# Kernel tuning notes

Measured on AMD Instinct MI355X. Metric: run time of the kernel, lower is better.

## Reference

```python
import jax, jax.numpy as jnp
import numpy as np

D_MODEL = 256
N_HEADS = 8
N_LEVELS = 4
N_POINTS = 4
HEAD_DIM = D_MODEL // N_HEADS
SPATIAL = [(64, 64), (32, 32), (16, 16), (8, 8)]
LEN_IN = sum(h * w for h, w in SPATIAL)
BATCH = 4
LEN_Q = LEN_IN


def _offset_bias():
    # replicate the module's _reset_parameters grid init for sampling_offsets.bias
    th = np.arange(N_HEADS, dtype=np.float64) * (2.0 * np.pi / N_HEADS)
    g = np.stack([np.cos(th), np.sin(th)], -1)
    g = g / np.abs(g).max(-1, keepdims=True)
    g = np.tile(g[:, None, None, :], (1, N_LEVELS, N_POINTS, 1))
    g = g * (np.arange(N_POINTS) + 1)[None, None, :, None]
    return jnp.asarray(g.reshape(-1), jnp.float32)


def setup_inputs() -> dict:
    key = jax.random.key(0)
    ks = jax.random.split(key, 10)
    s = 1.0 / np.sqrt(D_MODEL)
    return {
        "query": jax.random.normal(ks[0], (BATCH, LEN_Q, D_MODEL), jnp.float32),
        "reference_points": jax.random.uniform(ks[1], (BATCH, LEN_Q, N_LEVELS, 2), jnp.float32),
        "input_flatten": jax.random.normal(ks[2], (BATCH, LEN_IN, D_MODEL), jnp.float32),
        "input_spatial_shapes": np.array(SPATIAL, dtype=np.int64),
        "input_level_start_index": np.cumsum([0] + [h * w for h, w in SPATIAL[:-1]]).astype(np.int64),
        "W_val": jax.random.normal(ks[3], (D_MODEL, D_MODEL), jnp.float32) * s,
        "b_val": jnp.zeros((D_MODEL,), jnp.float32),
        "W_off": jax.random.normal(ks[4], (D_MODEL, N_HEADS * N_LEVELS * N_POINTS * 2), jnp.float32) * 0.01,
        "b_off": _offset_bias(),
        "W_attn": jax.random.normal(ks[5], (D_MODEL, N_HEADS * N_LEVELS * N_POINTS), jnp.float32) * 0.01,
        "b_attn": jnp.zeros((N_HEADS * N_LEVELS * N_POINTS,), jnp.float32),
        "W_out": jax.random.normal(ks[6], (D_MODEL, D_MODEL), jnp.float32) * s,
        "b_out": jnp.zeros((D_MODEL,), jnp.float32),
    }


def bilinear_sample(v, grid):
    # v: [B, C, H, W]; grid: [B, Q, P, 2] normalized to [-1, 1] (x=W axis, y=H axis)
    # matches torch F.grid_sample(mode='bilinear', padding_mode='zeros', align_corners=False)
    B, C, H, W = v.shape
    x = (grid[..., 0] + 1.0) * (W * 0.5) - 0.5
    y = (grid[..., 1] + 1.0) * (H * 0.5) - 0.5
    x0 = jnp.floor(x)
    y0 = jnp.floor(y)
    wx = x - x0
    wy = y - y0
    v_flat = v.reshape(B, C, H * W)

    def corner(xi, yi, wgt):
        valid = (xi >= 0) & (xi <= W - 1) & (yi >= 0) & (yi <= H - 1)
        xc = jnp.clip(xi, 0, W - 1).astype(jnp.int32)
        yc = jnp.clip(yi, 0, H - 1).astype(jnp.int32)
        idx = (yc * W + xc).reshape(B, 1, -1)
        g = jnp.take_along_axis(v_flat, jnp.broadcast_to(idx, (B, C, idx.shape[-1])), axis=2)
        return g * (wgt * valid).reshape(B, 1, -1)

    out = (corner(x0, y0, (1 - wx) * (1 - wy))
           + corner(x0 + 1, y0, wx * (1 - wy))
           + corner(x0, y0 + 1, (1 - wx) * wy)
           + corner(x0 + 1, y0 + 1, wx * wy))
    return out.reshape(B, C, grid.shape[1], grid.shape[2])


def reference(query, reference_points, input_flatten, input_spatial_shapes,
              input_level_start_index, W_val, b_val, W_off, b_off,
              W_attn, b_attn, W_out, b_out):
    ss = np.asarray(input_spatial_shapes)  # static [L, 2] (H, W)
    Nb, Lq, _ = query.shape
    value = (input_flatten @ W_val + b_val).reshape(Nb, -1, N_HEADS, HEAD_DIM)
    off = (query @ W_off + b_off).reshape(Nb, Lq, N_HEADS, N_LEVELS, N_POINTS, 2)
    attn = (query @ W_attn + b_attn).reshape(Nb, Lq, N_HEADS, N_LEVELS * N_POINTS)
    attn = jax.nn.softmax(attn, -1).reshape(Nb, Lq, N_HEADS, N_LEVELS, N_POINTS)
    # offset normalizer: (W, H) per level
    normalizer = jnp.asarray(ss[:, ::-1].copy(), jnp.float32)
    loc = reference_points[:, :, None, :, None, :] + off / normalizer[None, None, None, :, None, :]
    grids = 2.0 * loc - 1.0  # [N, Lq, H, L, P, 2]
    splits = np.cumsum([int(h) * int(w) for h, w in ss])[:-1]
    value_list = jnp.split(value, splits, axis=1)
    out = jnp.zeros((Nb * N_HEADS, HEAD_DIM, Lq), query.dtype)
    for lid, (h, w) in enumerate(ss):
        h, w = int(h), int(w)
        v = value_list[lid].transpose(0, 2, 3, 1).reshape(Nb * N_HEADS, HEAD_DIM, h, w)
        g = grids[:, :, :, lid].transpose(0, 2, 1, 3, 4).reshape(Nb * N_HEADS, Lq, N_POINTS, 2)
        sampled = bilinear_sample(v, g)  # [N*H, D, Lq, P]
        aw = attn[:, :, :, lid].transpose(0, 2, 1, 3).reshape(Nb * N_HEADS, 1, Lq, N_POINTS)
        out = out + (sampled * aw).sum(-1)
    out = out.reshape(Nb, N_HEADS * HEAD_DIM, Lq).transpose(0, 2, 1)
    return out @ W_out + b_out
```

## Files before the change

### kernel.cpp

```cpp
#include <hip/hip_runtime.h>
#include <hip/hip_bf16.h>
#include <math.h>

typedef unsigned short ushort_t;
typedef __attribute__((ext_vector_type(8))) short bf16x8;
typedef __attribute__((ext_vector_type(4))) float f32x4;
typedef __attribute__((ext_vector_type(2))) float f32x2;

constexpr int BATCH   = 4;
constexpr int D_MODEL = 256;
constexpr int LEN_IN  = 5440;
constexpr int LEN_Q   = 5440;
constexpr int M_TOT   = BATCH * LEN_Q;

#define ASG __attribute__((address_space(1)))
#define ASL __attribute__((address_space(3)))

__device__ __forceinline__ void gld16(const void* g, void* l) {
    __builtin_amdgcn_global_load_lds((ASG const void*)g, (ASL void*)l, 16, 0, 0);
}

__device__ __forceinline__ ushort_t bfbits(float x) {
    __hip_bfloat16 h = __float2bfloat16(x);
    ushort_t u; __builtin_memcpy(&u, &h, 2); return u;
}
__device__ __forceinline__ unsigned pk2(float a, float b) {
    return (unsigned)bfbits(a) | ((unsigned)bfbits(b) << 16);
}

__global__ __launch_bounds__(256) void pack_weights(
    const float* __restrict__ Wv, const float* __restrict__ Wout,
    const float* __restrict__ Wo, const float* __restrict__ Wa,
    const float* __restrict__ b_off, const float* __restrict__ b_attn,
    ushort_t* __restrict__ wvT, ushort_t* __restrict__ woutT,
    ushort_t* __restrict__ woaT, float* __restrict__ bias_oa)
{
    const int blk = blockIdx.x, t = threadIdx.x;
    if (blk < 64) {
        const float* src = (blk < 32) ? Wv : Wout;
        ushort_t*    dst = (blk < 32) ? wvT : woutT;
        const int k0 = (blk & 31) * 8;
        float f[8];
#pragma unroll
        for (int i = 0; i < 8; i++) f[i] = src[(k0 + i) * 256 + t];
        *(uint4*)(dst + t * 256 + k0) =
            make_uint4(pk2(f[0], f[1]), pk2(f[2], f[3]),
                       pk2(f[4], f[5]), pk2(f[6], f[7]));
    } else if (blk < 96) {
        const int k0 = (blk - 64) * 8;
#pragma unroll
        for (int rep = 0; rep < 2; rep++) {
            const int j = (rep == 0) ? t : 256 + t;
            if (rep == 1 && t >= 128) break;
            float f[8];
#pragma unroll
            for (int i = 0; i < 8; i++)
                f[i] = (j < 256) ? Wo[(k0 + i) * 256 + j]
                                 : Wa[(k0 + i) * 128 + (j - 256)];
            *(uint4*)(woaT + j * 256 + k0) =
                make_uint4(pk2(f[0], f[1]), pk2(f[2], f[3]),
                           pk2(f[4], f[5]), pk2(f[6], f[7]));
        }
    } else {
        bias_oa[t] = b_off[t];
        if (t < 128) bias_oa[256 + t] = b_attn[t];
    }
}

template <int OUT_MODE, bool A_F32, int NB>
__device__ __forceinline__ void gemm_core(
    const void* __restrict__ Ap, const ushort_t* __restrict__ BT,
    const float* __restrict__ bias, void* __restrict__ Cp, int N,
    int bm, int bn, ushort_t* As, ushort_t* Bs)
{
    const int tid  = threadIdx.x;
    const int wave = tid >> 6, lane = tid & 63;
    const int wm = (wave >> 1) * 64, wn = (wave & 1) * 64;
    const int c0 = 2 * wave, c1 = 2 * wave + 1;
    const int kb = (lane & 3) * 8;
    const int ar0 = bm + c0 * 16 + (lane >> 2);
    const int ar1 = bm + c1 * 16 + (lane >> 2);
    const ushort_t* gA0h = nullptr; const ushort_t* gA1h = nullptr;
    const float*    gA0f = nullptr; const float*    gA1f = nullptr;
    if (A_F32) {
        gA0f = (const float*)Ap + (size_t)ar0 * 256 + kb;
        gA1f = (const float*)Ap + (size_t)ar1 * 256 + kb;
    } else {
        gA0h = (const ushort_t*)Ap + (size_t)ar0 * 256 + kb;
        gA1h = (const ushort_t*)Ap + (size_t)ar1 * 256 + kb;
    }
    const ushort_t* gB0[NB]; const ushort_t* gB1[NB];
    ushort_t* lB0[NB]; ushort_t* lB1[NB];
#pragma unroll
    for (int nb = 0; nb < NB; nb++) {
        gB0[nb] = BT + (size_t)(bn + nb * 128 + c0 * 16 + (lane >> 2)) * 256 + kb;
        gB1[nb] = BT + (size_t)(bn + nb * 128 + c1 * 16 + (lane >> 2)) * 256 + kb;
        lB0[nb] = Bs + nb * 4096 + c0 * 512;
        lB1[nb] = Bs + nb * 4096 + c1 * 512;
    }
    ushort_t* lA0 = As + c0 * 512;
    ushort_t* lA1 = As + c1 * 512;

    f32x4 acc[NB][4][4] = {};
    const int row = lane & 15, kg = (lane >> 4) * 8;
    for (int kt = 0; kt < 8; kt++) {
        if (A_F32) {
            float4 a0 = *(const float4*)gA0f;
            float4 a1 = *(const float4*)(gA0f + 4);
            float4 b0 = *(const float4*)gA1f;
            float4 b1 = *(const float4*)(gA1f + 4);
            *(uint4*)(lA0 + lane * 8) =
                make_uint4(pk2(a0.x, a0.y), pk2(a0.z, a0.w),
                           pk2(a1.x, a1.y), pk2(a1.z, a1.w));
            *(uint4*)(lA1 + lane * 8) =
                make_uint4(pk2(b0.x, b0.y), pk2(b0.z, b0.w),
                           pk2(b1.x, b1.y), pk2(b1.z, b1.w));
            gA0f += 32; gA1f += 32;
        } else {
            gld16(gA0h, lA0); gld16(gA1h, lA1);
            gA0h += 32; gA1h += 32;
        }
#pragma unroll
        for (int nb = 0; nb < NB; nb++) {
            gld16(gB0[nb], lB0[nb]); gld16(gB1[nb], lB1[nb]);
            gB0[nb] += 32; gB1[nb] += 32;
        }
        __syncthreads();
        bf16x8 af[4];
#pragma unroll
        for (int i = 0; i < 4; i++)
            af[i] = *(const bf16x8*)(As + (wm + i * 16 + row) * 32 + kg);
#pragma unroll
        for (int nb = 0; nb < NB; nb++) {
            bf16x8 bfr[4];
#pragma unroll
            for (int j = 0; j < 4; j++)
                bfr[j] = *(const bf16x8*)(Bs + nb * 4096 + (wn + j * 16 + row) * 32 + kg);
#pragma unroll
            for (int i = 0; i < 4; i++)
#pragma unroll
                for (int j = 0; j < 4; j++)
                    acc[nb][i][j] = __builtin_amdgcn_mfma_f32_16x16x32_bf16(
                        af[i], bfr[j], acc[nb][i][j], 0, 0, 0);
        }
        __syncthreads();
    }

    const int col = lane & 15, rbase = (lane >> 4) * 4;
#pragma unroll
    for (int nb = 0; nb < NB; nb++) {
#pragma unroll
        for (int j = 0; j < 4; j++) {
            const int cc = bn + nb * 128 + wn + j * 16 + col;
            const float bv = bias[cc];
#pragma unroll
            for (int i = 0; i < 4; i++) {
                const int rr = bm + wm + i * 16 + rbase;
#pragma unroll
                for (int r = 0; r < 4; r++) {
                    const float v = acc[nb][i][j][r] + bv;
                    const int m = rr + r;
                    if (OUT_MODE == 0) {
                        ((float*)Cp)[(size_t)m * N + cc] = v;
                    } else {
                        const int bb  = m / LEN_IN;
                        const int pix = m - bb * LEN_IN;
                        const int head = cc >> 5, ch = cc & 31;
                        ((ushort_t*)Cp)[((size_t)((bb * 8 + head) * LEN_IN + pix) << 5) + ch] = bfbits(v);
                    }
                }
            }
        }
    }
}

__global__ __launch_bounds__(256) void gemm_dual(
    const float* __restrict__ inflat, const ushort_t* __restrict__ wvT,
    const float* __restrict__ b_val, ushort_t* __restrict__ value_bf,
    const float* __restrict__ query, const ushort_t* __restrict__ woaT,
    const float* __restrict__ bias_oa, float* __restrict__ offattn)
{
    __shared__ ushort_t As[128 * 32];
    __shared__ ushort_t Bs[2 * 128 * 32];
    const int blk = blockIdx.x;
    if (blk < 170) {
        gemm_core<2, true, 2>(inflat, wvT, b_val, value_bf, 256,
                              blk * 128, 0, As, Bs);
    } else if (blk < 340) {
        gemm_core<0, true, 2>(query, woaT, bias_oa, offattn, 384,
                              (blk - 170) * 128, 0, As, Bs);
    } else {
        gemm_core<0, true, 1>(query, woaT, bias_oa, offattn, 384,
                              (blk - 340) * 128, 256, As, Bs);
    }
}

__global__ __launch_bounds__(256) void gemm_out(
    const ushort_t* __restrict__ mid_bf, const ushort_t* __restrict__ woutT,
    const float* __restrict__ b_out, float* __restrict__ out)
{
    __shared__ ushort_t As[128 * 32];
    __shared__ ushort_t Bs[128 * 32];
    const int bn = (blockIdx.x & 1) * 128, bm = (blockIdx.x >> 1) * 128;
    gemm_core<0, false, 1>(mid_bf, woutT, b_out, out, 256, bm, bn, As, Bs);
}

__device__ __forceinline__ void accd(f32x2& a, unsigned u, f32x2 w) {
    f32x2 v;
    v.x = __uint_as_float(u << 16);
    v.y = __uint_as_float(u & 0xFFFF0000u);
    a = w * v + a;
}
__device__ __forceinline__ void accp(f32x2* a, uint4 u, float wf) {
    const f32x2 w = {wf, wf};
    accd(a[0], u.x, w); accd(a[1], u.y, w);
    accd(a[2], u.z, w); accd(a[3], u.w, w);
}

__global__ __launch_bounds__(256) void msda_sample_v4(
    const ushort_t* __restrict__ value,
    const float* __restrict__ refp,
    const float* __restrict__ offattn,
    ushort_t* __restrict__ mid)
{
    __shared__ float4 wLDS[64][16];
    __shared__ float4 aLDS[64][16];
    __shared__ float  esLDS[64];

    const int tid = threadIdx.x;
    const unsigned bid = blockIdx.x;
    const int xcd   = bid & 7;
    const int pos   = bid >> 3;
    const int slice = pos / 85;
    const int qc    = pos - slice * 85;
    const int bh    = xcd * 4 + slice;
    const int b     = bh >> 3, h = bh & 7;
    const int bqbase = b * LEN_Q + qc * 64;

    {
        const int p  = tid & 15;
        const int qg = tid >> 4;
        const int l  = p >> 2;
        const int shift = 6 - l;
        const int W  = 1 << shift;
        const float fW   = (float)W;
        const float invW = __uint_as_float((unsigned)(127 - shift) << 23);
        const int st = (l == 0) ? 0 : (l == 1) ? 4096 : (l == 2) ? 5120 : 5376;

#pragma unroll
        for (int it = 0; it < 4; it++) {
            const int ql = it * 16 + qg;
            const int bq = bqbase + ql;
            const float* oab = offattn + (size_t)bq * 384;
            const float2 off = *(const float2*)(oab + h * 32 + p * 2);
            const float  lgv = oab[256 + h * 16 + p];
            const float2 rl  = *(const float2*)(refp + (size_t)bq * 8 + l * 2);

            float mx = lgv;
            mx = fmaxf(mx, __shfl_xor(mx, 1));
            mx = fmaxf(mx, __shfl_xor(mx, 2));
            mx = fmaxf(mx, __shfl_xor(mx, 4));
            mx = fmaxf(mx, __shfl_xor(mx, 8));
            const float e = __expf(lgv - mx);
            float es = e;
            es += __shfl_xor(es, 1);
            es += __shfl_xor(es, 2);
            es += __shfl_xor(es, 4);
            es += __shfl_xor(es, 8);

            const float x = (rl.x + off.x * invW) * fW - 0.5f;
            const float y = (rl.y + off.y * invW) * fW - 0.5f;
            const float x0f = floorf(x), y0f = floorf(y);
            const float wx = x - x0f, wy = y - y0f;
            const int ix0 = (int)x0f, iy0 = (int)y0f;
            const int ix1 = ix0 + 1,  iy1 = iy0 + 1;
            const float vx0 = (ix0 >= 0 && ix0 < W) ? 1.f : 0.f;
            const float vx1 = (ix1 >= 0 && ix1 < W) ? 1.f : 0.f;
            const float vy0 = (iy0 >= 0 && iy0 < W) ? 1.f : 0.f;
            const float vy1 = (iy1 >= 0 && iy1 < W) ? 1.f : 0.f;
            const int cx0 = min(max(ix0, 0), W - 1);
            const int cx1 = min(max(ix1, 0), W - 1);
            const int cy0 = min(max(iy0, 0), W - 1);
            const int cy1 = min(max(iy1, 0), W - 1);
            const float hx0 = (1.f - wx) * vx0, hx1 = wx * vx1;
            const float hy0 = (1.f - wy) * vy0, hy1 = wy * vy1;

            const int off00 = (st + (cy0 << shift) + cx0) << 6;
            const int dxB   = (cx1 - cx0) << 6;
            const int dyB   = ((cy1 - cy0) << shift) << 6;

            const int ps = p ^ (ql & 15);
            wLDS[ql][ps] = make_float4(e * hx0 * hy0, e * hx1 * hy0,
                                       e * hx0 * hy1, e * hx1 * hy1);
            aLDS[ql][ps] = make_float4(__int_as_float(off00), __int_as_float(dxB),
                                       __int_as_float(dyB), 0.f);
            if (p == 0) esLDS[ql] = es;
        }
    }
    __syncthreads();

    const int ql = tid >> 2;
    const int cg = tid & 3;
    const int bq = bqbase + ql;
    const char* vb = (const char*)value + (size_t)bh * (LEN_IN * 64) + cg * 16;
    const float inv = 1.f / esLDS[ql];
    const int qs = ql & 15;

    f32x2 acc2[4];
#pragma unroll
    for (int d = 0; d < 4; d++) acc2[d] = (f32x2){0.f, 0.f};

#pragma unroll
    for (int pp = 0; pp < 16; pp++) {
        const float4 w  = wLDS[ql][pp ^ qs];
        const float4 ai = aLDS[ql][pp ^ qs];
        const int o00 = __float_as_int(ai.x);
        const int dx  = __float_as_int(ai.y);
        const int dy  = __float_as_int(ai.z);
        const char* c00 = vb + o00;
        uint4 v00 = *(const uint4*)(c00);
        uint4 v01 = *(const uint4*)(c00 + dx);
        uint4 v10 = *(const uint4*)(c00 + dy);
        uint4 v11 = *(const uint4*)(c00 + dx + dy);
        accp(acc2, v00, w.x);
        accp(acc2, v01, w.y);
        accp(acc2, v10, w.z);
        accp(acc2, v11, w.w);
    }

    uint4 o;
    o.x = pk2(acc2[0].x * inv, acc2[0].y * inv);
    o.y = pk2(acc2[1].x * inv, acc2[1].y * inv);
    o.z = pk2(acc2[2].x * inv, acc2[2].y * inv);
    o.w = pk2(acc2[3].x * inv, acc2[3].y * inv);
    ((uint4*)(mid + (size_t)bq * 256 + h * 32))[cg] = o;
}

extern "C" void kernel_launch(void* const* d_in, const int* in_sizes, int n_in,
                              void* d_out, int out_size, void* d_ws, size_t ws_size,
                              hipStream_t stream)
{
    const float* query  = (const float*)d_in[0];
    const float* refp   = (const float*)d_in[1];
    const float* inflat = (const float*)d_in[2];
    const float* W_val  = (const float*)d_in[5];
    const float* b_val  = (const float*)d_in[6];
    const float* W_off  = (const float*)d_in[7];
    const float* W_attn = (const float*)d_in[9];
    const float* b_off  = (const float*)d_in[8];
    const float* b_attn = (const float*)d_in[10];
    const float* W_out  = (const float*)d_in[11];
    const float* b_out  = (const float*)d_in[12];
    float* out = (float*)d_out;

    char* ws = (char*)d_ws;
    ushort_t* mid_bf   = (ushort_t*)ws;
    ushort_t* value_bf = (ushort_t*)(ws + 11141120);
    ushort_t* wvT      = (ushort_t*)(ws + 22282240);
    ushort_t* woutT    = (ushort_t*)(ws + 22413312);
    ushort_t* woaT     = (ushort_t*)(ws + 22544384);
    float*    bias_oa  = (float*)   (ws + 22740992);
    float*    offattn  = (float*)   (ws + 22742528);

    dim3 blk(256);
    pack_weights<<<dim3(97), blk, 0, stream>>>(
        W_val, W_out, W_off, W_attn, b_off, b_attn,
        wvT, woutT, woaT, bias_oa);
    gemm_dual<<<dim3(510), blk, 0, stream>>>(
        inflat, wvT, b_val, value_bf, query, woaT, bias_oa, offattn);
    msda_sample_v4<<<dim3(2720), blk, 0, stream>>>(
        value_bf, refp, offattn, mid_bf);
    gemm_out<<<dim3(340), blk, 0, stream>>>(
        mid_bf, woutT, b_out, out);
}
```

Before: 176.7 us.

## Double-buffer GEMM LDS tiles and pack sampler offsets into int2

The shared GEMM core now keeps two LDS buffers for the A and B tiles. It issues the loads for k-tile kt+1 before the MFMA work on tile kt, so global-to-LDS traffic overlaps with compute. This doubles LDS use per block (to 48 KB in gemm_dual), which may lower occupancy. Separately, the sampling kernel stores its per-point corner offsets as an int2, packing dx and dy into 16-bit halves instead of a float4, which cuts LDS footprint and read bandwidth.

Result: no change. 176.0 us (-0.4%).

```diff
diff --git a/kernel.cpp b/kernel.cpp
--- a/kernel.cpp
+++ b/kernel.cpp
@@ -90,52 +90,60 @@
         gA1h = (const ushort_t*)Ap + (size_t)ar1 * 256 + kb;
     }
     const ushort_t* gB0[NB]; const ushort_t* gB1[NB];
-    ushort_t* lB0[NB]; ushort_t* lB1[NB];
 #pragma unroll
     for (int nb = 0; nb < NB; nb++) {
         gB0[nb] = BT + (size_t)(bn + nb * 128 + c0 * 16 + (lane >> 2)) * 256 + kb;
         gB1[nb] = BT + (size_t)(bn + nb * 128 + c1 * 16 + (lane >> 2)) * 256 + kb;
-        lB0[nb] = Bs + nb * 4096 + c0 * 512;
-        lB1[nb] = Bs + nb * 4096 + c1 * 512;
-    }
-    ushort_t* lA0 = As + c0 * 512;
-    ushort_t* lA1 = As + c1 * 512;
+    }
+
+    auto STAGE = [&](int kt, int buf) {
+        ushort_t* as = As + buf * 4096;
+        ushort_t* bs = Bs + buf * (NB * 4096);
+        if (A_F32) {
+            const float* a0 = gA0f + kt * 32;
+            const float* a1 = gA1f + kt * 32;
+            float4 x0 = *(const float4*)a0;
+            float4 x1 = *(const float4*)(a0 + 4);
+            float4 y0 = *(const float4*)a1;
+            float4 y1 = *(const float4*)(a1 + 4);
+            *(uint4*)(as + c0 * 512 + lane * 8) =
+                make_uint4(pk2(x0.x, x0.y), pk2(x0.z, x0.w),
+                           pk2(x1.x, x1.y), pk2(x1.z, x1.w));
+            *(uint4*)(as + c1 * 512 + lane * 8) =
+                make_uint4(pk2(y0.x, y0.y), pk2(y0.z, y0.w),
+                           pk2(y1.x, y1.y), pk2(y1.z, y1.w));
+        } else {
+            gld16(gA0h + kt * 32, as + c0 * 512);
+            gld16(gA1h + kt * 32, as + c1 * 512);
+        }
+#pragma unroll
+        for (int nb = 0; nb < NB; nb++) {
+            gld16(gB0[nb] + kt * 32, bs + nb * 4096 + c0 * 512);
+            gld16(gB1[nb] + kt * 32, bs + nb * 4096 + c1 * 512);
+        }
+    };
 
     f32x4 acc[NB][4][4] = {};
     const int row = lane & 15, kg = (lane >> 4) * 8;
+
+    STAGE(0, 0);
+    __syncthreads();
+
     for (int kt = 0; kt < 8; kt++) {
-        if (A_F32) {
-            float4 a0 = *(const float4*)gA0f;
-            float4 a1 = *(const float4*)(gA0f + 4);
-            float4 b0 = *(const float4*)gA1f;
-            float4 b1 = *(const float4*)(gA1f + 4);
-            *(uint4*)(lA0 + lane * 8) =
-                make_uint4(pk2(a0.x, a0.y), pk2(a0.z, a0.w),
-                           pk2(a1.x, a1.y), pk2(a1.z, a1.w));
-            *(uint4*)(lA1 + lane * 8) =
-                make_uint4(pk2(b0.x, b0.y), pk2(b0.z, b0.w),
-                           pk2(b1.x, b1.y), pk2(b1.z, b1.w));
-            gA0f += 32; gA1f += 32;
-        } else {
-            gld16(gA0h, lA0); gld16(gA1h, lA1);
-            gA0h += 32; gA1h += 32;
-        }
-#pragma unroll
-        for (int nb = 0; nb < NB; nb++) {
-            gld16(gB0[nb], lB0[nb]); gld16(gB1[nb], lB1[nb]);
-            gB0[nb] += 32; gB1[nb] += 32;
-        }
-        __syncthreads();
+        const int cur = kt & 1;
+        if (kt < 7) STAGE(kt + 1, cur ^ 1);
+        const ushort_t* as = As + cur * 4096;
+        const ushort_t* bs = Bs + cur * (NB * 4096);
         bf16x8 af[4];
 #pragma unroll
         for (int i = 0; i < 4; i++)
-            af[i] = *(const bf16x8*)(As + (wm + i * 16 + row) * 32 + kg);
+            af[i] = *(const bf16x8*)(as + (wm + i * 16 + row) * 32 + kg);
 #pragma unroll
         for (int nb = 0; nb < NB; nb++) {
             bf16x8 bfr[4];
 #pragma unroll
             for (int j = 0; j < 4; j++)
-                bfr[j] = *(const bf16x8*)(Bs + nb * 4096 + (wn + j * 16 + row) * 32 + kg);
+                bfr[j] = *(const bf16x8*)(bs + nb * 4096 + (wn + j * 16 + row) * 32 + kg);
 #pragma unroll
             for (int i = 0; i < 4; i++)
 #pragma unroll
@@ -180,8 +188,8 @@
     const float* __restrict__ query, const ushort_t* __restrict__ woaT,
     const float* __restrict__ bias_oa, float* __restrict__ offattn)
 {
-    __shared__ ushort_t As[128 * 32];
-    __shared__ ushort_t Bs[2 * 128 * 32];
+    __shared__ ushort_t As[2 * 128 * 32];
+    __shared__ ushort_t Bs[2 * 2 * 128 * 32];
     const int blk = blockIdx.x;
     if (blk < 170) {
         gemm_core<2, true, 2>(inflat, wvT, b_val, value_bf, 256,
@@ -199,8 +207,8 @@
     const ushort_t* __restrict__ mid_bf, const ushort_t* __restrict__ woutT,
     const float* __restrict__ b_out, float* __restrict__ out)
 {
-    __shared__ ushort_t As[128 * 32];
-    __shared__ ushort_t Bs[128 * 32];
+    __shared__ ushort_t As[2 * 128 * 32];
+    __shared__ ushort_t Bs[2 * 128 * 32];
     const int bn = (blockIdx.x & 1) * 128, bm = (blockIdx.x >> 1) * 128;
     gemm_core<0, false, 1>(mid_bf, woutT, b_out, out, 256, bm, bn, As, Bs);
 }
@@ -224,7 +232,7 @@
     ushort_t* __restrict__ mid)
 {
     __shared__ float4 wLDS[64][16];
-    __shared__ float4 aLDS[64][16];
+    __shared__ int2   aLDS[64][16];
     __shared__ float  esLDS[64];
 
     const int tid = threadIdx.x;
@@ -292,8 +300,7 @@
             const int ps = p ^ (ql & 15);
             wLDS[ql][ps] = make_float4(e * hx0 * hy0, e * hx1 * hy0,
                                        e * hx0 * hy1, e * hx1 * hy1);
-            aLDS[ql][ps] = make_float4(__int_as_float(off00), __int_as_float(dxB),
-                                       __int_as_float(dyB), 0.f);
+            aLDS[ql][ps] = make_int2(off00, (dxB << 16) | dyB);
             if (p == 0) esLDS[ql] = es;
         }
     }
@@ -313,10 +320,10 @@
 #pragma unroll
     for (int pp = 0; pp < 16; pp++) {
         const float4 w  = wLDS[ql][pp ^ qs];
-        const float4 ai = aLDS[ql][pp ^ qs];
-        const int o00 = __float_as_int(ai.x);
-        const int dx  = __float_as_int(ai.y);
-        const int dy  = __float_as_int(ai.z);
+        const int2   ai = aLDS[ql][pp ^ qs];
+        const int o00 = ai.x;
+        const int dx  = ai.y >> 16;
+        const int dy  = ai.y & 0xFFFF;
         const char* c00 = vb + o00;
         uint4 v00 = *(const uint4*)(c00);
         uint4 v01 = *(const uint4*)(c00 + dx);
```
